# Kernel tuning notes

Hardware: AMD Instinct MI355X
Metric: run time of the kernel (lower is better)

## Reference

```python
import jax, jax.numpy as jnp
import numpy as np

N = 1048576
BINS = 32
HID = 64
OUT = 64
IN_DIMS = 7


def setup_inputs() -> dict:
    key = jax.random.key(0)
    ks = jax.random.split(key, 9)
    pos01 = jax.random.uniform(ks[0], (N, 3), dtype=jnp.float32)
    wi01 = jax.random.uniform(ks[1], (N, 3), dtype=jnp.float32)
    rough01 = jax.random.uniform(ks[2], (N, 1), dtype=jnp.float32)
    enc_dim = IN_DIMS * BINS  # 224
    W1 = jax.random.normal(ks[3], (enc_dim, HID), dtype=jnp.float32) / np.sqrt(enc_dim)
    b1 = jnp.zeros((HID,), dtype=jnp.float32)
    W2 = jax.random.normal(ks[4], (HID, HID), dtype=jnp.float32) / np.sqrt(HID)
    b2 = jnp.zeros((HID,), dtype=jnp.float32)
    W3 = jax.random.normal(ks[5], (HID, OUT), dtype=jnp.float32) / np.sqrt(HID)
    b3 = jnp.zeros((OUT,), dtype=jnp.float32)
    centers = jnp.linspace(0.0, 1.0, BINS, dtype=jnp.float32)
    return {"pos01": pos01, "wi01": wi01, "rough01": rough01,
            "W1": W1, "b1": b1, "W2": W2, "b2": b2, "W3": W3, "b3": b3,
            "centers": centers}


def reference(pos01, wi01, rough01, W1, b1, W2, b2, W3, b3, centers):
    # Concatenate + clamp to [0,1]: [N, 7]
    x = jnp.clip(jnp.concatenate([pos01, wi01, rough01], axis=1), 0.0, 1.0)
    sigma = 1.0 / BINS
    # OneBlob gaussian encoding: [N, 7, BINS] -> [N, 7*BINS]
    diff = x[:, :, None] - centers[None, None, :]
    enc = jnp.exp(-0.5 * (diff / sigma) ** 2).reshape(x.shape[0], -1)
    # 3-layer MLP with ReLU
    h = jax.nn.relu(enc @ W1 + b1)
    h = jax.nn.relu(h @ W2 + b2)
    return h @ W3 + b3
```

## Files before the change

kernel.cpp:

```cpp
#include <hip/hip_runtime.h>

typedef __bf16 bf16x8 __attribute__((ext_vector_type(8)));
typedef float  f32x4  __attribute__((ext_vector_type(4)));

constexpr int HID = 64;
constexpr float K1   = 27.178297f;
constexpr float STEP = -K1 / 31.0f;


__global__ void prep_kernel(const float* __restrict__ W1,
                            const float* __restrict__ W2,
                            const float* __restrict__ W3,
                            bf16x8* __restrict__ ws)
{
    const int f = blockIdx.x;
    const int l = threadIdx.x;
    const int g = l >> 4, r = l & 15;
    bf16x8 v;
    if (f < 28) {
        const int kk = f >> 2, mt = f & 3;
#pragma unroll
        for (int j = 0; j < 8; ++j)
            v[j] = (__bf16)W1[(32 * kk + 8 * g + j) * HID + 16 * mt + r];
    } else {
        const float* W = (f < 36) ? W2 : W3;
        const int fi = (f < 36) ? (f - 28) : (f - 36);
        const int mt = fi >> 1, kk2 = fi & 1;
#pragma unroll
        for (int j = 0; j < 8; ++j) {
            const int k = 32 * kk2 + 16 * (j >> 2) + 4 * g + (j & 3);
            v[j] = (__bf16)W[k * HID + 16 * mt + r];
        }
    }
    ws[f * 64 + l] = v;
}

__device__ __forceinline__ void load_x(const float* __restrict__ pos,
                                       const float* __restrict__ wi,
                                       const float* __restrict__ rough,
                                       int row, float* x)
{
    x[0] = pos[row * 3 + 0]; x[1] = pos[row * 3 + 1]; x[2] = pos[row * 3 + 2];
    x[3] = wi[row * 3 + 0];  x[4] = wi[row * 3 + 1];  x[5] = wi[row * 3 + 2];
    x[6] = rough[row];
}

__device__ __forceinline__ void mlp_tail(const f32x4* acc1, const char* lb,
                                         const f32x4* b2v, const f32x4* b3v,
                                         float* __restrict__ out, int row, int g)
{
    bf16x8 h1f[2];
#pragma unroll
    for (int kk2 = 0; kk2 < 2; ++kk2) {
        bf16x8 v;
#pragma unroll
        for (int j = 0; j < 8; ++j)
            v[j] = (__bf16)fmaxf(acc1[2 * kk2 + (j >> 2)][j & 3], 0.0f);
        h1f[kk2] = v;
    }
    f32x4 acc2[4];
#pragma unroll
    for (int mt = 0; mt < 4; ++mt) acc2[mt] = b2v[mt];
#pragma unroll
    for (int kk2 = 0; kk2 < 2; ++kk2)
#pragma unroll
        for (int mt = 0; mt < 4; ++mt) {
            const bf16x8 wf = *(const bf16x8*)(lb + (28 + mt * 2 + kk2) * 1024);
            acc2[mt] = __builtin_amdgcn_mfma_f32_16x16x32_bf16(wf, h1f[kk2], acc2[mt], 0, 0, 0);
        }

    bf16x8 h2f[2];
#pragma unroll
    for (int kk2 = 0; kk2 < 2; ++kk2) {
        bf16x8 v;
#pragma unroll
        for (int j = 0; j < 8; ++j)
            v[j] = (__bf16)fmaxf(acc2[2 * kk2 + (j >> 2)][j & 3], 0.0f);
        h2f[kk2] = v;
    }
    f32x4 acc3[4];
#pragma unroll
    for (int mt = 0; mt < 4; ++mt) acc3[mt] = b3v[mt];
#pragma unroll
    for (int kk2 = 0; kk2 < 2; ++kk2)
#pragma unroll
        for (int mt = 0; mt < 4; ++mt) {
            const bf16x8 wf = *(const bf16x8*)(lb + (36 + mt * 2 + kk2) * 1024);
            acc3[mt] = __builtin_amdgcn_mfma_f32_16x16x32_bf16(wf, h2f[kk2], acc3[mt], 0, 0, 0);
        }
#pragma unroll
    for (int mt = 0; mt < 4; ++mt)
        __builtin_nontemporal_store(acc3[mt],
            (f32x4*)(out + (size_t)row * 64 + 16 * mt + 4 * g));
}

__global__ __launch_bounds__(512, 4)
void cond_net_kernel(const float* __restrict__ pos, const float* __restrict__ wi,
                     const float* __restrict__ rough,
                     const float* __restrict__ b1, const float* __restrict__ b2,
                     const float* __restrict__ b3,
                     const bf16x8* __restrict__ ws,
                     float* __restrict__ out)
{
    __shared__ bf16x8 wlds[44 * 64];

    const int tid = threadIdx.x;
    const int l = tid & 63, wv = tid >> 6, g = l >> 4, r = l & 15;

    for (int fr = wv; fr < 44; fr += 8)
        __builtin_amdgcn_global_load_lds(
            (const __attribute__((address_space(1))) void*)(ws + fr * 64 + l),
            (__attribute__((address_space(3))) void*)(wlds + fr * 64),
            16, 0, 0);

    f32x4 b1v[4], b2v[4], b3v[4];
#pragma unroll
    for (int mt = 0; mt < 4; ++mt) {
        b1v[mt] = *(const f32x4*)(b1 + 16 * mt + 4 * g);
        b2v[mt] = *(const f32x4*)(b2 + 16 * mt + 4 * g);
        b3v[mt] = *(const f32x4*)(b3 + 16 * mt + 4 * g);
    }

    const float base_g = STEP * (float)(8 * g);
    const int rbase = blockIdx.x * 1024 + wv * 32 + r;

    float xc[14];
    load_x(pos, wi, rough, rbase, xc);
    load_x(pos, wi, rough, rbase + 16, xc + 7);

    __syncthreads();

    unsigned int ldsoff = 0;
#pragma unroll 1
    for (int it = 0; it < 4; ++it) {
        asm volatile("" : "+v"(ldsoff));
        const char* lb = (const char*)wlds + ldsoff + l * 16;

        float xn[14];
        const int nrow = rbase + (it < 3 ? (it + 1) * 256 : 768);
        load_x(pos, wi, rough, nrow, xn);
        load_x(pos, wi, rough, nrow + 16, xn + 7);

        float Aa[7], Ab[7];
#pragma unroll
        for (int d = 0; d < 7; ++d) {
            Aa[d] = fmaf(K1, fminf(fmaxf(xc[d], 0.0f), 1.0f), base_g);
            Ab[d] = fmaf(K1, fminf(fmaxf(xc[7 + d], 0.0f), 1.0f), base_g);
        }

        f32x4 accA[4], accB[4];
#pragma unroll
        for (int mt = 0; mt < 4; ++mt) { accA[mt] = b1v[mt]; accB[mt] = b1v[mt]; }

#pragma unroll
        for (int kk = 0; kk < 7; ++kk) {
            bf16x8 e0, e1;
#pragma unroll
            for (int j = 0; j < 8; ++j) {
                const float d0 = Aa[kk] + (float)j * STEP;
                const float d1 = Ab[kk] + (float)j * STEP;
                e0[j] = (__bf16)__builtin_amdgcn_exp2f(-(d0 * d0));
                e1[j] = (__bf16)__builtin_amdgcn_exp2f(-(d1 * d1));
            }
#pragma unroll
            for (int mt = 0; mt < 4; ++mt) {
                const bf16x8 wf = *(const bf16x8*)(lb + (kk * 4 + mt) * 1024);
                accA[mt] = __builtin_amdgcn_mfma_f32_16x16x32_bf16(wf, e0, accA[mt], 0, 0, 0);
                accB[mt] = __builtin_amdgcn_mfma_f32_16x16x32_bf16(wf, e1, accB[mt], 0, 0, 0);
            }
        }

        const int row0 = rbase + it * 256;
        mlp_tail(accA, lb, b2v, b3v, out, row0, g);
        mlp_tail(accB, lb, b2v, b3v, out, row0 + 16, g);

#pragma unroll
        for (int q = 0; q < 14; ++q) xc[q] = xn[q];
    }
}

extern "C" void kernel_launch(void* const* d_in, const int* in_sizes, int n_in,
                              void* d_out, int out_size, void* d_ws, size_t ws_size,
                              hipStream_t stream) {
    const float* pos     = (const float*)d_in[0];
    const float* wi      = (const float*)d_in[1];
    const float* rough   = (const float*)d_in[2];
    const float* W1      = (const float*)d_in[3];
    const float* b1      = (const float*)d_in[4];
    const float* W2      = (const float*)d_in[5];
    const float* b2      = (const float*)d_in[6];
    const float* W3      = (const float*)d_in[7];
    const float* b3      = (const float*)d_in[8];
    float* out = (float*)d_out;

    bf16x8* ws = (bf16x8*)d_ws;

    const int n = in_sizes[0] / 3;
    hipLaunchKernelGGL(prep_kernel, dim3(44), dim3(64), 0, stream, W1, W2, W3, ws);
    hipLaunchKernelGGL(cond_net_kernel, dim3(n / 1024), dim3(512), 0, stream,
                       pos, wi, rough, b1, b2, b3, (const bf16x8*)ws, out);
}
```

Measured before the change: 85.23 us.

## Compute Gaussian encoding by recurrence, interleave MLP tails, double rows per block

Each 8-bin Gaussian group now costs two exp2 calls plus a multiplicative recurrence (exp of a shifted square expands into geometric factors) instead of eight exp2 calls. The two 16-row MLP tails are interleaved so their independent MFMA chains can overlap. Each block now processes 2048 rows over 8 iterations, which halves the grid and amortises the weight-to-LDS load. The recurrence can build up rounding error across the eight bins, and the larger blocks leave fewer of them to spread over the CUs.

New measurement: 99.18 us. +16.4%, slower.

```diff
diff --git a/kernel.cpp b/kernel.cpp
--- a/kernel.cpp
+++ b/kernel.cpp
@@ -6,6 +6,9 @@
 constexpr int HID = 64;
 constexpr float K1   = 27.178297f;
 constexpr float STEP = -K1 / 31.0f;
+constexpr float M2STEP = -2.0f * STEP;
+constexpr float NSTEP2 = -STEP * STEP;
+constexpr float WMUL   = 0.34453753f;
 
 
 __global__ void prep_kernel(const float* __restrict__ W1,
@@ -45,53 +48,19 @@
     x[6] = rough[row];
 }
 
-__device__ __forceinline__ void mlp_tail(const f32x4* acc1, const char* lb,
-                                         const f32x4* b2v, const f32x4* b3v,
-                                         float* __restrict__ out, int row, int g)
-{
-    bf16x8 h1f[2];
-#pragma unroll
-    for (int kk2 = 0; kk2 < 2; ++kk2) {
-        bf16x8 v;
-#pragma unroll
-        for (int j = 0; j < 8; ++j)
-            v[j] = (__bf16)fmaxf(acc1[2 * kk2 + (j >> 2)][j & 3], 0.0f);
-        h1f[kk2] = v;
-    }
-    f32x4 acc2[4];
-#pragma unroll
-    for (int mt = 0; mt < 4; ++mt) acc2[mt] = b2v[mt];
-#pragma unroll
-    for (int kk2 = 0; kk2 < 2; ++kk2)
-#pragma unroll
-        for (int mt = 0; mt < 4; ++mt) {
-            const bf16x8 wf = *(const bf16x8*)(lb + (28 + mt * 2 + kk2) * 1024);
-            acc2[mt] = __builtin_amdgcn_mfma_f32_16x16x32_bf16(wf, h1f[kk2], acc2[mt], 0, 0, 0);
-        }
-
-    bf16x8 h2f[2];
-#pragma unroll
-    for (int kk2 = 0; kk2 < 2; ++kk2) {
-        bf16x8 v;
-#pragma unroll
-        for (int j = 0; j < 8; ++j)
-            v[j] = (__bf16)fmaxf(acc2[2 * kk2 + (j >> 2)][j & 3], 0.0f);
-        h2f[kk2] = v;
-    }
-    f32x4 acc3[4];
-#pragma unroll
-    for (int mt = 0; mt < 4; ++mt) acc3[mt] = b3v[mt];
-#pragma unroll
-    for (int kk2 = 0; kk2 < 2; ++kk2)
-#pragma unroll
-        for (int mt = 0; mt < 4; ++mt) {
-            const bf16x8 wf = *(const bf16x8*)(lb + (36 + mt * 2 + kk2) * 1024);
-            acc3[mt] = __builtin_amdgcn_mfma_f32_16x16x32_bf16(wf, h2f[kk2], acc3[mt], 0, 0, 0);
-        }
-#pragma unroll
-    for (int mt = 0; mt < 4; ++mt)
-        __builtin_nontemporal_store(acc3[mt],
-            (f32x4*)(out + (size_t)row * 64 + 16 * mt + 4 * g));
+__device__ __forceinline__ bf16x8 enc8(float a)
+{
+    bf16x8 e;
+    float u = __builtin_amdgcn_exp2f(-(a * a));
+    float v = __builtin_amdgcn_exp2f(fmaf(a, M2STEP, NSTEP2));
+    e[0] = (__bf16)u;
+#pragma unroll
+    for (int j = 1; j < 8; ++j) {
+        u *= v;
+        v *= WMUL;
+        e[j] = (__bf16)u;
+    }
+    return e;
 }
 
 __global__ __launch_bounds__(512, 4)
@@ -102,7 +71,7 @@
                      const bf16x8* __restrict__ ws,
                      float* __restrict__ out)
 {
-    __shared__ bf16x8 wlds[44 * 64];
+    __shared__ __align__(16) char lds[44 * 1024];
 
     const int tid = threadIdx.x;
     const int l = tid & 63, wv = tid >> 6, g = l >> 4, r = l & 15;
@@ -110,7 +79,7 @@
     for (int fr = wv; fr < 44; fr += 8)
         __builtin_amdgcn_global_load_lds(
             (const __attribute__((address_space(1))) void*)(ws + fr * 64 + l),
-            (__attribute__((address_space(3))) void*)(wlds + fr * 64),
+            (__attribute__((address_space(3))) void*)(lds + fr * 1024),
             16, 0, 0);
 
     f32x4 b1v[4], b2v[4], b3v[4];
@@ -122,7 +91,7 @@
     }
 
     const float base_g = STEP * (float)(8 * g);
-    const int rbase = blockIdx.x * 1024 + wv * 32 + r;
+    const int rbase = blockIdx.x * 2048 + wv * 32 + r;
 
     float xc[14];
     load_x(pos, wi, rough, rbase, xc);
@@ -132,12 +101,12 @@
 
     unsigned int ldsoff = 0;
 #pragma unroll 1
-    for (int it = 0; it < 4; ++it) {
+    for (int it = 0; it < 8; ++it) {
         asm volatile("" : "+v"(ldsoff));
-        const char* lb = (const char*)wlds + ldsoff + l * 16;
+        const char* lb = (const char*)lds + ldsoff + l * 16;
 
         float xn[14];
-        const int nrow = rbase + (it < 3 ? (it + 1) * 256 : 768);
+        const int nrow = rbase + ((it + 1) & 7) * 256;
         load_x(pos, wi, rough, nrow, xn);
         load_x(pos, wi, rough, nrow + 16, xn + 7);
 
@@ -154,14 +123,8 @@
 
 #pragma unroll
         for (int kk = 0; kk < 7; ++kk) {
-            bf16x8 e0, e1;
-#pragma unroll
-            for (int j = 0; j < 8; ++j) {
-                const float d0 = Aa[kk] + (float)j * STEP;
-                const float d1 = Ab[kk] + (float)j * STEP;
-                e0[j] = (__bf16)__builtin_amdgcn_exp2f(-(d0 * d0));
-                e1[j] = (__bf16)__builtin_amdgcn_exp2f(-(d1 * d1));
-            }
+            const bf16x8 e0 = enc8(Aa[kk]);
+            const bf16x8 e1 = enc8(Ab[kk]);
 #pragma unroll
             for (int mt = 0; mt < 4; ++mt) {
                 const bf16x8 wf = *(const bf16x8*)(lb + (kk * 4 + mt) * 1024);
@@ -170,9 +133,62 @@
             }
         }
 
+        bf16x8 h1fA[2], h1fB[2];
+#pragma unroll
+        for (int kk2 = 0; kk2 < 2; ++kk2) {
+            bf16x8 va, vb;
+#pragma unroll
+            for (int j = 0; j < 8; ++j) {
+                va[j] = (__bf16)fmaxf(accA[2 * kk2 + (j >> 2)][j & 3], 0.0f);
+                vb[j] = (__bf16)fmaxf(accB[2 * kk2 + (j >> 2)][j & 3], 0.0f);
+            }
+            h1fA[kk2] = va; h1fB[kk2] = vb;
+        }
+
+        f32x4 acc2A[4], acc2B[4];
+#pragma unroll
+        for (int mt = 0; mt < 4; ++mt) { acc2A[mt] = b2v[mt]; acc2B[mt] = b2v[mt]; }
+#pragma unroll
+        for (int kk2 = 0; kk2 < 2; ++kk2)
+#pragma unroll
+            for (int mt = 0; mt < 4; ++mt) {
+                const bf16x8 wf = *(const bf16x8*)(lb + (28 + mt * 2 + kk2) * 1024);
+                acc2A[mt] = __builtin_amdgcn_mfma_f32_16x16x32_bf16(wf, h1fA[kk2], acc2A[mt], 0, 0, 0);
+                acc2B[mt] = __builtin_amdgcn_mfma_f32_16x16x32_bf16(wf, h1fB[kk2], acc2B[mt], 0, 0, 0);
+            }
+
+        bf16x8 h2fA[2], h2fB[2];
+#pragma unroll
+        for (int kk2 = 0; kk2 < 2; ++kk2) {
+            bf16x8 va, vb;
+#pragma unroll
+            for (int j = 0; j < 8; ++j) {
+                va[j] = (__bf16)fmaxf(acc2A[2 * kk2 + (j >> 2)][j & 3], 0.0f);
+                vb[j] = (__bf16)fmaxf(acc2B[2 * kk2 + (j >> 2)][j & 3], 0.0f);
+            }
+            h2fA[kk2] = va; h2fB[kk2] = vb;
+        }
+
+        f32x4 acc3A[4], acc3B[4];
+#pragma unroll
+        for (int mt = 0; mt < 4; ++mt) { acc3A[mt] = b3v[mt]; acc3B[mt] = b3v[mt]; }
+#pragma unroll
+        for (int kk2 = 0; kk2 < 2; ++kk2)
+#pragma unroll
+            for (int mt = 0; mt < 4; ++mt) {
+                const bf16x8 wf = *(const bf16x8*)(lb + (36 + mt * 2 + kk2) * 1024);
+                acc3A[mt] = __builtin_amdgcn_mfma_f32_16x16x32_bf16(wf, h2fA[kk2], acc3A[mt], 0, 0, 0);
+                acc3B[mt] = __builtin_amdgcn_mfma_f32_16x16x32_bf16(wf, h2fB[kk2], acc3B[mt], 0, 0, 0);
+            }
+
         const int row0 = rbase + it * 256;
-        mlp_tail(accA, lb, b2v, b3v, out, row0, g);
-        mlp_tail(accB, lb, b2v, b3v, out, row0 + 16, g);
+#pragma unroll
+        for (int mt = 0; mt < 4; ++mt) {
+            __builtin_nontemporal_store(acc3A[mt],
+                (f32x4*)(out + (size_t)row0 * 64 + 16 * mt + 4 * g));
+            __builtin_nontemporal_store(acc3B[mt],
+                (f32x4*)(out + (size_t)(row0 + 16) * 64 + 16 * mt + 4 * g));
+        }
 
 #pragma unroll
         for (int q = 0; q < 14; ++q) xc[q] = xn[q];
@@ -197,6 +213,6 @@
 
     const int n = in_sizes[0] / 3;
     hipLaunchKernelGGL(prep_kernel, dim3(44), dim3(64), 0, stream, W1, W2, W3, ws);
-    hipLaunchKernelGGL(cond_net_kernel, dim3(n / 1024), dim3(512), 0, stream,
+    hipLaunchKernelGGL(cond_net_kernel, dim3(n / 2048), dim3(512), 0, stream,
                        pos, wi, rough, b1, b2, b3, (const bf16x8*)ws, out);
 }
```
